# Optimization experiments

Measured on AMD Instinct MI355X. Metric: run time of the kernel, lower is better.

## Reference

```python
import jax, jax.numpy as jnp
import numpy as np

EPS = 1e-5
DN = ('NCHW', 'OIHW', 'NCHW')


def _conv3x3(x, w):
    return jax.lax.conv_general_dilated(x, w, (1, 1), 'SAME', dimension_numbers=DN)


def _bn_relu(x, g, b):
    # eval-mode BN: running_mean=0, running_var=1
    scale = (g / jnp.sqrt(1.0 + EPS))[None, :, None, None]
    return jax.nn.relu(x * scale + b[None, :, None, None])


def _double_conv(x, w1, g1, b1, w2, g2, b2):
    x = _bn_relu(_conv3x3(x, w1), g1, b1)
    return _bn_relu(_conv3x3(x, w2), g2, b2)


def _up2x_bilinear_align(x):
    # bilinear, align_corners=True, scale_factor=2
    def interp(a, axis, n_in):
        n_out = 2 * n_in
        pos = jnp.arange(n_out, dtype=jnp.float32) * (n_in - 1) / (n_out - 1)
        lo = jnp.floor(pos).astype(jnp.int32)
        hi = jnp.minimum(lo + 1, n_in - 1)
        w = pos - lo.astype(jnp.float32)
        sh = [1, 1, 1, 1]
        sh[axis] = n_out
        w = w.reshape(sh)
        return jnp.take(a, lo, axis=axis) * (1.0 - w) + jnp.take(a, hi, axis=axis) * w
    B, C, H, W = x.shape
    return interp(interp(x, 2, H), 3, W)


def _lstm_dir(seq, Wih, Whh, bih, bhh, reverse):
    # seq: (N, T, C) -> (N, T, Hh); PyTorch gate order i,f,g,o
    Hh = Whh.shape[1]
    xg = jnp.einsum('ntc,gc->ntg', seq, Wih) + (bih + bhh)
    if reverse:
        xg = xg[:, ::-1]
    xg = jnp.swapaxes(xg, 0, 1)  # (T, N, 4H)
    N = seq.shape[0]
    h0 = jnp.zeros((N, Hh), seq.dtype)

    def step(carry, gx):
        h, c = carry
        g = gx + h @ Whh.T
        i, f, gg, o = jnp.split(g, 4, axis=-1)
        c = jax.nn.sigmoid(f) * c + jax.nn.sigmoid(i) * jnp.tanh(gg)
        h = jax.nn.sigmoid(o) * jnp.tanh(c)
        return (h, c), h

    _, hs = jax.lax.scan(step, (h0, h0), xg)
    hs = jnp.swapaxes(hs, 0, 1)  # (N, T, Hh)
    if reverse:
        hs = hs[:, ::-1]
    return hs


def _bilstm(seq, Wf, Uf, bif, bhf, Wb, Ub, bib, bhb):
    return jnp.concatenate([
        _lstm_dir(seq, Wf, Uf, bif, bhf, False),
        _lstm_dir(seq, Wb, Ub, bib, bhb, True),
    ], axis=-1)


def _site_rows(x, lstm):
    # batched version of per-row LSTM: each row is a sequence over W, features C
    B, C, H, W = x.shape
    s = jnp.transpose(x, (0, 2, 3, 1)).reshape(B * H, W, C)
    out = _bilstm(s, *lstm)  # (B*H, W, C) since 2*hidden == C
    return jnp.transpose(out.reshape(B, H, W, C), (0, 3, 1, 2))


def _site_cols(x, lstm):
    # each column is a sequence over H, features C
    B, C, H, W = x.shape
    s = jnp.transpose(x, (0, 3, 2, 1)).reshape(B * W, H, C)
    out = _bilstm(s, *lstm)
    return jnp.transpose(out.reshape(B, W, H, C), (0, 3, 2, 1))


def setup_inputs() -> dict:
    key = jax.random.key(0)
    ks = jax.random.split(key, 24)
    d = {}
    d['x1'] = jax.random.normal(ks[0], (8, 128, 32, 32), jnp.float32)
    d['x2'] = jax.random.normal(ks[1], (8, 128, 64, 64), jnp.float32)
    # bidirectional LSTM: input 256, hidden 128
    d['lstm_Wih_f'] = jax.random.normal(ks[2], (512, 256), jnp.float32) * 0.06
    d['lstm_Whh_f'] = jax.random.normal(ks[3], (512, 128), jnp.float32) * 0.08
    d['lstm_bih_f'] = jax.random.normal(ks[4], (512,), jnp.float32) * 0.05
    d['lstm_bhh_f'] = jax.random.normal(ks[5], (512,), jnp.float32) * 0.05
    d['lstm_Wih_b'] = jax.random.normal(ks[6], (512, 256), jnp.float32) * 0.06
    d['lstm_Whh_b'] = jax.random.normal(ks[7], (512, 128), jnp.float32) * 0.08
    d['lstm_bib_tmp'] = None
    del d['lstm_bib_tmp']
    d['lstm_bih_b'] = jax.random.normal(ks[8], (512,), jnp.float32) * 0.05
    d['lstm_bhh_b'] = jax.random.normal(ks[9], (512,), jnp.float32) * 0.05
    # conv_2 = DoubleConv(512, 256) (mid=256), shared across its two call sites
    d['c2_w1'] = jax.random.normal(ks[10], (256, 512, 3, 3), jnp.float32) * 0.02
    d['c2_g1'] = jax.random.uniform(ks[11], (256,), jnp.float32, 0.5, 1.5)
    d['c2_b1'] = jax.random.normal(ks[12], (256,), jnp.float32) * 0.05
    d['c2_w2'] = jax.random.normal(ks[13], (256, 256, 3, 3), jnp.float32) * 0.03
    d['c2_g2'] = jax.random.uniform(ks[14], (256,), jnp.float32, 0.5, 1.5)
    d['c2_b2'] = jax.random.normal(ks[15], (256,), jnp.float32) * 0.05
    # conv = DoubleConv(256, 128, mid=128)
    d['cv_w1'] = jax.random.normal(ks[16], (128, 256, 3, 3), jnp.float32) * 0.03
    d['cv_g1'] = jax.random.uniform(ks[17], (128,), jnp.float32, 0.5, 1.5)
    d['cv_b1'] = jax.random.normal(ks[18], (128,), jnp.float32) * 0.05
    d['cv_w2'] = jax.random.normal(ks[19], (128, 128, 3, 3), jnp.float32) * 0.04
    d['cv_g2'] = jax.random.uniform(ks[20], (128,), jnp.float32, 0.5, 1.5)
    d['cv_b2'] = jax.random.normal(ks[21], (128,), jnp.float32) * 0.05
    return d


def reference(x1, x2, lstm_Wih_f, lstm_Whh_f, lstm_bih_f, lstm_bhh_f,
              lstm_Wih_b, lstm_Whh_b, lstm_bih_b, lstm_bhh_b,
              c2_w1, c2_g1, c2_b1, c2_w2, c2_g2, c2_b2,
              cv_w1, cv_g1, cv_b1, cv_w2, cv_g2, cv_b2):
    lstm = (lstm_Wih_f, lstm_Whh_f, lstm_bih_f, lstm_bhh_f,
            lstm_Wih_b, lstm_Whh_b, lstm_bih_b, lstm_bhh_b)
    x1u = _up2x_bilinear_align(x1)
    dy = x2.shape[2] - x1u.shape[2]
    dx = x2.shape[3] - x1u.shape[3]
    x1u = jnp.pad(x1u, ((0, 0), (0, 0), (dy // 2, dy - dy // 2), (dx // 2, dx - dx // 2)))
    x = jnp.concatenate([x2, x1u], axis=1)  # (B, 256, 64, 64)
    # site_relation mutates x in-place in torch: rows pass, then cols pass on the
    # row-updated tensor; x_weigth and x_heigth alias the same final tensor.
    x = _site_rows(x, lstm)
    x = _site_cols(x, lstm)
    x_site = jnp.concatenate([x, x], axis=1)  # (B, 512, H, W)
    x_site = _double_conv(x_site, c2_w1, c2_g1, c2_b1, c2_w2, c2_g2, c2_b2)
    x = jnp.concatenate([x, x_site], axis=1)  # (B, 512, H, W)
    x = _double_conv(x, c2_w1, c2_g1, c2_b1, c2_w2, c2_g2, c2_b2)
    x = _double_conv(x, cv_w1, cv_g1, cv_b1, cv_w2, cv_g2, cv_b2)
    return x  # (B, 128, 64, 64)
```

## Files before the change

### kernel.cpp

```cpp
#include <hip/hip_runtime.h>
#include <hip/hip_bf16.h>
#include <math.h>

typedef __bf16 bf16x8 __attribute__((ext_vector_type(8)));
typedef float  f32x4  __attribute__((ext_vector_type(4)));

__device__ __forceinline__ float sigm(float x)  { return 1.f/(1.f+__expf(-x)); }
__device__ __forceinline__ float tanh_f(float x){ return 2.f/(1.f+__expf(-2.f*x)) - 1.f; }
__device__ __forceinline__ float b2f(unsigned short u){
  unsigned int x = ((unsigned int)u) << 16; return __uint_as_float(x);
}
__device__ __forceinline__ unsigned short f2b(float v){
  __hip_bfloat16 h = __float2bfloat16(v); return *(unsigned short*)&h;
}
__device__ __forceinline__ void glds16(const void* g, void* l) {
  __builtin_amdgcn_global_load_lds(
      (const __attribute__((address_space(1))) unsigned int*)g,
      (__attribute__((address_space(3))) unsigned int*)l, 16, 0, 0);
}
__device__ __forceinline__ bf16x8 bzero() {
  bf16x8 v;
  #pragma unroll
  for (int i = 0; i < 8; ++i) v[i] = (__bf16)0.0f;
  return v;
}
__device__ __forceinline__ void barrier_lds() {
  asm volatile("s_waitcnt lgkmcnt(0)\n\ts_barrier" ::: "memory");
}

__global__ __launch_bounds__(256) void k_upcat(const float* __restrict__ x1,
                                               const float* __restrict__ x2,
                                               __hip_bfloat16* __restrict__ X0) {
  int idx = blockIdx.x*256 + threadIdx.x;
  int c = idx & 255;
  int w = (idx >> 8) & 63;
  int h = (idx >> 14) & 63;
  int n = idx >> 20;
  float v;
  if (c < 128) {
    v = x2[((n*128 + c)*64 + h)*64 + w];
  } else {
    int cc = c - 128;
    float py = (h*31.0f)/63.0f;
    int ly = (int)py; int hy = min(ly+1, 31); float fy = py - (float)ly;
    float px = (w*31.0f)/63.0f;
    int lx = (int)px; int hx = min(lx+1, 31); float fx = px - (float)lx;
    const float* p = x1 + (size_t)(n*128 + cc)*1024;
    float v00 = p[ly*32+lx], v01 = p[ly*32+hx];
    float v10 = p[hy*32+lx], v11 = p[hy*32+hx];
    v = (1.f-fy)*((1.f-fx)*v00 + fx*v01) + fy*((1.f-fx)*v10 + fx*v11);
  }
  X0[idx] = __float2bfloat16(v);
}

__global__ __launch_bounds__(256) void k_wih_prep(
    const float* __restrict__ Wf, const float* __restrict__ Wb,
    const float* __restrict__ bif, const float* __restrict__ bhf,
    const float* __restrict__ bib, const float* __restrict__ bhb,
    __hip_bfloat16* __restrict__ wihc, float* __restrict__ biasc) {
  int idx = blockIdx.x*256 + threadIdx.x;
  int n = idx >> 8, k = idx & 255;
  float v = (n < 512) ? Wf[n*256 + k] : Wb[(n-512)*256 + k];
  wihc[idx] = __float2bfloat16(v);
  if (idx < 1024) biasc[idx] = (idx < 512) ? bif[idx] + bhf[idx]
                                           : bib[idx-512] + bhb[idx-512];
}

__global__ __launch_bounds__(256) void k_xg_gemm(
    const __hip_bfloat16* __restrict__ Xin,
    const __hip_bfloat16* __restrict__ Wihc,
    const float* __restrict__ biasc,
    __hip_bfloat16* __restrict__ xg) {
  __shared__ __align__(16) unsigned short sa[128][72];
  __shared__ __align__(16) unsigned short sw[128][72];
  int bx = blockIdx.x;
  int t = bx >> 2, seq0 = (bx & 3) << 7;
  int n0 = blockIdx.y << 7;
  int tid = threadIdx.x, lane = tid & 63, wid = tid >> 6;
  int wm = wid >> 1, wn = wid & 1;
  int l15 = lane & 15, quad = lane >> 4;
  f32x4 acc[4][4];
  #pragma unroll
  for (int i = 0; i < 4; ++i)
    #pragma unroll
    for (int j = 0; j < 4; ++j) acc[i][j] = (f32x4){0.f,0.f,0.f,0.f};

  for (int k0 = 0; k0 < 256; k0 += 64) {
    __syncthreads();
    for (int idx = tid; idx < 2048; idx += 256) {
      int row = idx >> 4, c4 = (idx & 15) << 2;
      *(ushort4*)&sa[row][c4] = *(const ushort4*)((const unsigned short*)Xin +
          (size_t)((seq0 + row)*64 + t)*256 + k0 + c4);
      *(ushort4*)&sw[row][c4] = *(const ushort4*)((const unsigned short*)Wihc +
          (size_t)(n0 + row)*256 + k0 + c4);
    }
    __syncthreads();
    #pragma unroll
    for (int k32 = 0; k32 < 64; k32 += 32) {
      bf16x8 af[4], bfr[4];
      #pragma unroll
      for (int mt = 0; mt < 4; ++mt)
        af[mt] = *(const bf16x8*)&sa[wm*64 + mt*16 + l15][k32 + quad*8];
      #pragma unroll
      for (int nt = 0; nt < 4; ++nt)
        bfr[nt] = *(const bf16x8*)&sw[wn*64 + nt*16 + l15][k32 + quad*8];
      #pragma unroll
      for (int mt = 0; mt < 4; ++mt)
        #pragma unroll
        for (int nt = 0; nt < 4; ++nt)
          acc[mt][nt] = __builtin_amdgcn_mfma_f32_16x16x32_bf16(
              af[mt], bfr[nt], acc[mt][nt], 0, 0, 0);
    }
  }
  #pragma unroll
  for (int nt = 0; nt < 4; ++nt) {
    int cg = n0 + wn*64 + nt*16 + l15;
    int dir = cg >> 9;
    int g   = (cg >> 7) & 3;
    int u   = cg & 127;
    float bias = biasc[cg];
    unsigned short* op = (unsigned short*)xg +
        (size_t)(((dir*64 + t)*4 + g)*512)*128 + u;
    #pragma unroll
    for (int mt = 0; mt < 4; ++mt) {
      int sbase = seq0 + wm*64 + mt*16 + quad*4;
      f32x4 a = acc[mt][nt];
      #pragma unroll
      for (int r = 0; r < 4; ++r)
        op[(size_t)(sbase + r)*128] = f2b(a[r] + bias);
    }
  }
}

__global__ __launch_bounds__(256, 1) void k_lstm_rec(
    const __hip_bfloat16* __restrict__ xg,
    const float* __restrict__ WhhF, const float* __restrict__ WhhB,
    __hip_bfloat16* __restrict__ out) {
  const int dir = blockIdx.y;
  const int sb  = blockIdx.x;
  const float* Whh = dir ? WhhB : WhhF;
  __shared__ __align__(16) unsigned short hs[16][136];
  __shared__ __align__(16) float gv[4][128][4];
  const int tid = threadIdx.x, lane = tid & 63, wv = tid >> 6;
  const int l15 = lane & 15, quad = lane >> 4;

  bf16x8 wf[4][2][4];
  #pragma unroll
  for (int g = 0; g < 4; ++g)
    #pragma unroll
    for (int ut = 0; ut < 2; ++ut) {
      int gate = g*128 + wv*32 + ut*16 + l15;
      #pragma unroll
      for (int kc = 0; kc < 4; ++kc) {
        const float* wp = Whh + (size_t)gate*128 + kc*32 + quad*8;
        float4 w0 = *(const float4*)wp;
        float4 w1 = *(const float4*)(wp + 4);
        bf16x8 f;
        f[0]=(__bf16)w0.x; f[1]=(__bf16)w0.y; f[2]=(__bf16)w0.z; f[3]=(__bf16)w0.w;
        f[4]=(__bf16)w1.x; f[5]=(__bf16)w1.y; f[6]=(__bf16)w1.z; f[7]=(__bf16)w1.w;
        wf[g][ut][kc] = f;
      }
    }
  for (int i = tid; i < 16*136; i += 256) ((unsigned short*)hs)[i] = 0;

  const int u_  = tid & 127;
  const int s0_ = tid >> 7;
  float cst[2] = {0.f, 0.f};

  const unsigned short* xp = (const unsigned short*)xg +
      (size_t)dir*64*4*512*128;
  unsigned short xv[2][4], xn[2][4];
  #define LDX(stp, dst)                                                    \
    {                                                                      \
      int ts_ = (stp) < 64 ? (stp) : 63;                                   \
      int t_  = dir ? 63 - ts_ : ts_;                                      \
      _Pragma("unroll")                                                    \
      for (int j_ = 0; j_ < 2; ++j_) {                                     \
        int s_ = s0_ + j_*2;                                               \
        _Pragma("unroll")                                                  \
        for (int g_ = 0; g_ < 4; ++g_)                                     \
          dst[j_][g_] = xp[(size_t)((t_*4 + g_)*512 + sb*4 + s_)*128 + u_];\
      }                                                                    \
    }
  LDX(0, xv);
  __syncthreads();

  for (int step = 0; step < 64; ++step) {
    int t = dir ? 63 - step : step;
    LDX(step + 1, xn);
    bf16x8 af[2][4];
    #pragma unroll
    for (int mt = 0; mt < 2; ++mt)
      #pragma unroll
      for (int kc = 0; kc < 4; ++kc)
        af[mt][kc] = *(const bf16x8*)&hs[mt*16 + l15][kc*32 + quad*8];
    f32x4 acc[2][4][2];
    #pragma unroll
    for (int mt = 0; mt < 2; ++mt)
      #pragma unroll
      for (int g = 0; g < 4; ++g)
        #pragma unroll
        for (int ut = 0; ut < 2; ++ut) acc[mt][g][ut] = (f32x4){0.f,0.f,0.f,0.f};
    #pragma unroll
    for (int kc = 0; kc < 4; ++kc)
      #pragma unroll
      for (int mt = 0; mt < 2; ++mt)
        #pragma unroll
        for (int g = 0; g < 4; ++g)
          #pragma unroll
          for (int ut = 0; ut < 2; ++ut)
            acc[mt][g][ut] = __builtin_amdgcn_mfma_f32_16x16x32_bf16(
                af[mt][kc], wf[g][ut][kc], acc[mt][g][ut], 0, 0, 0);
    if (quad == 0) {
      #pragma unroll
      for (int ut = 0; ut < 2; ++ut) {
        int u = wv*32 + ut*16 + l15;
        #pragma unroll
        for (int r = 0; r < 4; ++r) {
          float4 q;
          q.x = acc[0][0][ut][r]; q.y = acc[0][1][ut][r];
          q.z = acc[0][2][ut][r]; q.w = acc[0][3][ut][r];
          *(float4*)&gv[r][u][0] = q;
        }
      }
    }
    barrier_lds();
    #pragma unroll
    for (int j = 0; j < 2; ++j) {
      int s = s0_ + j*2;
      float4 gq = *(const float4*)&gv[s][u_][0];
      float I = gq.x + b2f(xv[j][0]);
      float F = gq.y + b2f(xv[j][1]);
      float G = gq.z + b2f(xv[j][2]);
      float O = gq.w + b2f(xv[j][3]);
      float cv = sigm(F)*cst[j] + sigm(I)*tanh_f(G);
      float hv = sigm(O)*tanh_f(cv);
      cst[j] = cv;
      unsigned short hb = f2b(hv);
      hs[s][u_] = hb;
      int gs = sb*4 + s;
      ((unsigned short*)out)[(size_t)(((gs >> 6)*64 + t)*64 + (gs & 63))*256
                             + dir*128 + u_] = hb;
    }
    barrier_lds();
    #pragma unroll
    for (int j = 0; j < 2; ++j)
      #pragma unroll
      for (int g = 0; g < 4; ++g) xv[j][g] = xn[j][g];
  }
  #undef LDX
}

__global__ __launch_bounds__(256) void k_wrefmt_bf16(const float* __restrict__ src,
                                                     __hip_bfloat16* __restrict__ dst,
                                                     int Ci, int Co, int fold) {
  int idx = blockIdx.x*256 + threadIdx.x;
  int total = 9*Ci*Co;
  if (idx >= total) return;
  int ci = idx % Ci;
  int co = (idx / Ci) % Co;
  int k  = idx / (Ci*Co);
  int CiS = fold ? Ci*2 : Ci;
  float v = src[(size_t)(co*CiS + ci)*9 + k];
  if (fold) v += src[(size_t)(co*CiS + ci + Ci)*9 + k];
  dst[idx] = __float2bfloat16(v);
}

__global__ __launch_bounds__(256, 2) void k_conv3_v3(
    const __hip_bfloat16* __restrict__ inA, const __hip_bfloat16* __restrict__ inB,
    const __hip_bfloat16* __restrict__ wgt,
    const float* __restrict__ gam, const float* __restrict__ bet,
    float* __restrict__ outF, __hip_bfloat16* __restrict__ outB,
    int Cin, int Co, int nchw) {
  __shared__ __align__(16) unsigned short si[6][64][64];
  __shared__ __align__(16) unsigned short sw[3][64][64];
  int bx = blockIdx.x;
  int n  = bx >> 4;
  int h0 = (bx & 15) << 2;
  int co0 = blockIdx.y << 6;
  int tid = threadIdx.x;
  int lane = tid & 63;
  int wvid = tid >> 6;
  int l15 = lane & 15, quad = lane >> 4;
  int pl = lane >> 3, pc = lane & 7;

  f32x4 acc[4][4];
  #pragma unroll
  for (int i = 0; i < 4; ++i)
    #pragma unroll
    for (int j = 0; j < 4; ++j) acc[i][j] = (f32x4){0.f,0.f,0.f,0.f};

  int cs = inB ? 256 : Cin;
  for (int ci0 = 0; ci0 < Cin; ci0 += 64) {
    const unsigned short* src = (const unsigned short*)inA; int cb = ci0;
    if (inB && ci0 >= 256) { src = (const unsigned short*)inB; cb = ci0 - 256; }
    __syncthreads();
    #pragma unroll
    for (int j = 0; j < 12; ++j) {
      int s = wvid + j*4;
      int row = s >> 3, grp = s & 7;
      int ih = h0 + row - 1;
      if (ih >= 0 && ih <= 63) {
        const unsigned short* gsrc = src + (size_t)((n*64 + ih)*64)*cs + cb;
        int iw = grp*8 + pl;
        int lc = pc ^ (iw & 7);
        glds16(gsrc + (size_t)iw*cs + lc*8, &si[row][grp*8][0]);
      } else {
        uint4 z = {0,0,0,0};
        *(uint4*)((unsigned short*)&si[row][grp*8][0] + lane*8) = z;
      }
    }
    for (int ky = 0; ky < 3; ++ky) {
      if (ky) __syncthreads();
      {
        const unsigned short* wk = (const unsigned short*)wgt +
            (size_t)(ky*3*Co + co0)*Cin + ci0;
        #pragma unroll
        for (int j = 0; j < 6; ++j) {
          int s = wvid + j*4;
          int kx = s >> 3, cg = s & 7;
          int co = cg*8 + pl;
          int lc = pc ^ (co & 7);
          glds16(wk + (size_t)(kx*Co + co)*Cin + lc*8, &sw[kx][cg*8][0]);
        }
      }
      __syncthreads();
      int row = wvid + ky;
      #pragma unroll
      for (int kx = 0; kx < 3; ++kx) {
        #pragma unroll
        for (int k32 = 0; k32 < 2; ++k32) {
          bf16x8 af[4], bfr[4];
          #pragma unroll
          for (int mt = 0; mt < 4; ++mt) {
            int iw = mt*16 + l15 + kx - 1;
            int iwc = iw & 63;
            int pcc = (k32*4 + quad) ^ (iwc & 7);
            af[mt] = *(const bf16x8*)&si[row][iwc][pcc*8];
            if ((kx == 0 && mt == 0 && l15 == 0) ||
                (kx == 2 && mt == 3 && l15 == 15))
              af[mt] = bzero();
          }
          #pragma unroll
          for (int nt = 0; nt < 4; ++nt) {
            int co = nt*16 + l15;
            int pcc = (k32*4 + quad) ^ (co & 7);
            bfr[nt] = *(const bf16x8*)&sw[kx][co][pcc*8];
          }
          #pragma unroll
          for (int mt = 0; mt < 4; ++mt)
            #pragma unroll
            for (int nt = 0; nt < 4; ++nt)
              acc[mt][nt] = __builtin_amdgcn_mfma_f32_16x16x32_bf16(
                  af[mt], bfr[nt], acc[mt][nt], 0, 0, 0);
        }
      }
    }
  }
  const float kS = 0.9999950000374997f;
  int h = h0 + wvid;
  #pragma unroll
  for (int nt = 0; nt < 4; ++nt) {
    int co = co0 + nt*16 + l15;
    float scale = gam[co]*kS, bb = bet[co];
    #pragma unroll
    for (int mt = 0; mt < 4; ++mt) {
      f32x4 a = acc[mt][nt];
      #pragma unroll
      for (int r = 0; r < 4; ++r) {
        int w = mt*16 + quad*4 + r;
        float v = fmaf(a[r], scale, bb);
        v = v > 0.f ? v : 0.f;
        if (nchw) outF[(size_t)((n*Co + co)*64 + h)*64 + w] = v;
        else      outB[(size_t)((n*64 + h)*64 + w)*Co + co] = __float2bfloat16(v);
      }
    }
  }
}

extern "C" void kernel_launch(void* const* d_in, const int* in_sizes, int n_in,
                              void* d_out, int out_size, void* d_ws, size_t ws_size,
                              hipStream_t stream) {
  const float* x1    = (const float*)d_in[0];
  const float* x2    = (const float*)d_in[1];
  const float* Wih_f = (const float*)d_in[2];
  const float* Whh_f = (const float*)d_in[3];
  const float* bih_f = (const float*)d_in[4];
  const float* bhh_f = (const float*)d_in[5];
  const float* Wih_b = (const float*)d_in[6];
  const float* Whh_b = (const float*)d_in[7];
  const float* bih_b = (const float*)d_in[8];
  const float* bhh_b = (const float*)d_in[9];
  const float* c2_w1 = (const float*)d_in[10];
  const float* c2_g1 = (const float*)d_in[11];
  const float* c2_b1 = (const float*)d_in[12];
  const float* c2_w2 = (const float*)d_in[13];
  const float* c2_g2 = (const float*)d_in[14];
  const float* c2_b2 = (const float*)d_in[15];
  const float* cv_w1 = (const float*)d_in[16];
  const float* cv_g1 = (const float*)d_in[17];
  const float* cv_b1 = (const float*)d_in[18];
  const float* cv_w2 = (const float*)d_in[19];
  const float* cv_g2 = (const float*)d_in[20];
  const float* cv_b2 = (const float*)d_in[21];

  char* base = (char*)d_ws;
  const size_t SLOTB = 16777216ull;
  __hip_bfloat16* Xb  = (__hip_bfloat16*)(base);
  __hip_bfloat16* Sb  = (__hip_bfloat16*)(base);
  __hip_bfloat16* XG  = (__hip_bfloat16*)(base + SLOTB);
  __hip_bfloat16* D2  = (__hip_bfloat16*)(base + SLOTB);
  __hip_bfloat16* D2b = (__hip_bfloat16*)(base + 2*SLOTB);
  __hip_bfloat16* RT  = (__hip_bfloat16*)(base + SLOTB + 67108864ull);
  __hip_bfloat16* D1  = RT;
  char* wq = base + SLOTB + 67108864ull + SLOTB;
  __hip_bfloat16* wihc  = (__hip_bfloat16*)wq;
  float*          biasc = (float*)(wq + 524288);
  char* cw = wq + 528384;
  __hip_bfloat16* w1f    = (__hip_bfloat16*)(cw);
  __hip_bfloat16* w1full = (__hip_bfloat16*)(cw + 1179648);
  __hip_bfloat16* w2r    = (__hip_bfloat16*)(cw + 3538944);
  __hip_bfloat16* wv1    = (__hip_bfloat16*)(cw + 4718592);
  __hip_bfloat16* wv2    = (__hip_bfloat16*)(cw + 5308416);

  k_wih_prep<<<1024, 256, 0, stream>>>(Wih_f, Wih_b, bih_f, bhh_f, bih_b, bhh_b,
                                       wihc, biasc);
  k_wrefmt_bf16<<<(9*256*256+255)/256, 256, 0, stream>>>(c2_w1, w1f,    256, 256, 1);
  k_wrefmt_bf16<<<(9*512*256+255)/256, 256, 0, stream>>>(c2_w1, w1full, 512, 256, 0);
  k_wrefmt_bf16<<<(9*256*256+255)/256, 256, 0, stream>>>(c2_w2, w2r,    256, 256, 0);
  k_wrefmt_bf16<<<(9*256*128+255)/256, 256, 0, stream>>>(cv_w1, wv1,    256, 128, 0);
  k_wrefmt_bf16<<<(9*128*128+255)/256, 256, 0, stream>>>(cv_w2, wv2,    128, 128, 0);

  k_upcat<<<32768, 256, 0, stream>>>(x1, x2, Xb);

  k_xg_gemm<<<dim3(256, 8), 256, 0, stream>>>(Xb, wihc, biasc, XG);
  k_lstm_rec<<<dim3(128, 2), 256, 0, stream>>>(XG, Whh_f, Whh_b, RT);
  k_xg_gemm<<<dim3(256, 8), 256, 0, stream>>>(RT, wihc, biasc, XG);
  k_lstm_rec<<<dim3(128, 2), 256, 0, stream>>>(XG, Whh_f, Whh_b, Sb);

  k_conv3_v3<<<dim3(128,4), 256, 0, stream>>>(Sb, nullptr, w1f, c2_g1, c2_b1,
                                              nullptr, D1, 256, 256, 0);
  k_conv3_v3<<<dim3(128,4), 256, 0, stream>>>(D1, nullptr, w2r, c2_g2, c2_b2,
                                              nullptr, D2, 256, 256, 0);
  k_conv3_v3<<<dim3(128,4), 256, 0, stream>>>(Sb, D2, w1full, c2_g1, c2_b1,
                                              nullptr, D2b, 512, 256, 0);
  k_conv3_v3<<<dim3(128,4), 256, 0, stream>>>(D2b, nullptr, w2r, c2_g2, c2_b2,
                                              nullptr, D1, 256, 256, 0);
  k_conv3_v3<<<dim3(128,2), 256, 0, stream>>>(D1, nullptr, wv1, cv_g1, cv_b1,
                                              nullptr, D2, 256, 128, 0);
  k_conv3_v3<<<dim3(128,2), 256, 0, stream>>>(D2, nullptr, wv2, cv_g2, cv_b2,
                                              (float*)d_out, nullptr, 128, 128, 1);
}
```

Baseline: 656.8 us.

## Restructure LSTM recurrence: 16 sequences per block, transposed MFMA, double-buffered h

The recurrent LSTM kernel now handles 16 sequences per block instead of 4, so the grid shrinks from 128x2 to 32x2. The MFMA is transposed (weights as the A operand, h as B), which leaves each lane holding all four gate values for its units. The gate nonlinearities can then run straight from registers, with the input projection preloaded into the accumulator, dropping the LDS gate staging and one barrier per step. h is double-buffered in LDS so a single barrier per step suffices. The cost is fewer blocks (64 total) and therefore less parallelism on the device.

```diff
diff --git a/kernel.cpp b/kernel.cpp
--- a/kernel.cpp
+++ b/kernel.cpp
@@ -139,116 +139,116 @@
   const int dir = blockIdx.y;
   const int sb  = blockIdx.x;
   const float* Whh = dir ? WhhB : WhhF;
-  __shared__ __align__(16) unsigned short hs[16][136];
-  __shared__ __align__(16) float gv[4][128][4];
+  __shared__ __align__(16) unsigned short hs[2][16][136];
   const int tid = threadIdx.x, lane = tid & 63, wv = tid >> 6;
   const int l15 = lane & 15, quad = lane >> 4;
 
-  bf16x8 wf[4][2][4];
-  #pragma unroll
-  for (int g = 0; g < 4; ++g)
-    #pragma unroll
-    for (int ut = 0; ut < 2; ++ut) {
-      int gate = g*128 + wv*32 + ut*16 + l15;
+  bf16x8 wf[2][4][4];
+  #pragma unroll
+  for (int mt = 0; mt < 2; ++mt)
+    #pragma unroll
+    for (int g = 0; g < 4; ++g) {
+      int row = g*128 + wv*32 + mt*16 + l15;
       #pragma unroll
       for (int kc = 0; kc < 4; ++kc) {
-        const float* wp = Whh + (size_t)gate*128 + kc*32 + quad*8;
+        const float* wp = Whh + (size_t)row*128 + kc*32 + quad*8;
         float4 w0 = *(const float4*)wp;
         float4 w1 = *(const float4*)(wp + 4);
         bf16x8 f;
         f[0]=(__bf16)w0.x; f[1]=(__bf16)w0.y; f[2]=(__bf16)w0.z; f[3]=(__bf16)w0.w;
         f[4]=(__bf16)w1.x; f[5]=(__bf16)w1.y; f[6]=(__bf16)w1.z; f[7]=(__bf16)w1.w;
-        wf[g][ut][kc] = f;
+        wf[mt][g][kc] = f;
       }
     }
   for (int i = tid; i < 16*136; i += 256) ((unsigned short*)hs)[i] = 0;
 
-  const int u_  = tid & 127;
-  const int s0_ = tid >> 7;
-  float cst[2] = {0.f, 0.f};
-
+  const int seq = l15;
+  int xoff[2][4];
+  #pragma unroll
+  for (int mt = 0; mt < 2; ++mt)
+    #pragma unroll
+    for (int g = 0; g < 4; ++g)
+      xoff[mt][g] = ((g*512) + sb*16 + seq)*128 + wv*32 + mt*16 + quad*4;
   const unsigned short* xp = (const unsigned short*)xg +
       (size_t)dir*64*4*512*128;
-  unsigned short xv[2][4], xn[2][4];
-  #define LDX(stp, dst)                                                    \
-    {                                                                      \
-      int ts_ = (stp) < 64 ? (stp) : 63;                                   \
-      int t_  = dir ? 63 - ts_ : ts_;                                      \
-      _Pragma("unroll")                                                    \
-      for (int j_ = 0; j_ < 2; ++j_) {                                     \
-        int s_ = s0_ + j_*2;                                               \
-        _Pragma("unroll")                                                  \
-        for (int g_ = 0; g_ < 4; ++g_)                                     \
-          dst[j_][g_] = xp[(size_t)((t_*4 + g_)*512 + sb*4 + s_)*128 + u_];\
-      }                                                                    \
-    }
-  LDX(0, xv);
+  const int gs = sb*16 + seq;
+  unsigned short* outb = (unsigned short*)out +
+      ((size_t)(gs >> 6)*64)*64*256 + (size_t)(gs & 63)*256 + dir*128;
+
+  ushort4 xv[2][4], xn[2][4];
+  {
+    int t0 = dir ? 63 : 0;
+    const unsigned short* bt = xp + (size_t)t0*262144;
+    #pragma unroll
+    for (int mt = 0; mt < 2; ++mt)
+      #pragma unroll
+      for (int g = 0; g < 4; ++g)
+        xv[mt][g] = *(const ushort4*)(bt + xoff[mt][g]);
+  }
+  float cst[2][4];
+  #pragma unroll
+  for (int mt = 0; mt < 2; ++mt)
+    #pragma unroll
+    for (int r = 0; r < 4; ++r) cst[mt][r] = 0.f;
   __syncthreads();
 
-  for (int step = 0; step < 64; ++step) {
+  auto body = [&](int step, ushort4 (&xc)[2][4], ushort4 (&xf)[2][4]) {
     int t = dir ? 63 - step : step;
-    LDX(step + 1, xn);
-    bf16x8 af[2][4];
-    #pragma unroll
-    for (int mt = 0; mt < 2; ++mt)
-      #pragma unroll
-      for (int kc = 0; kc < 4; ++kc)
-        af[mt][kc] = *(const bf16x8*)&hs[mt*16 + l15][kc*32 + quad*8];
-    f32x4 acc[2][4][2];
-    #pragma unroll
-    for (int mt = 0; mt < 2; ++mt)
-      #pragma unroll
-      for (int g = 0; g < 4; ++g)
-        #pragma unroll
-        for (int ut = 0; ut < 2; ++ut) acc[mt][g][ut] = (f32x4){0.f,0.f,0.f,0.f};
-    #pragma unroll
-    for (int kc = 0; kc < 4; ++kc)
+    {
+      int sn = step + 1 < 64 ? step + 1 : 63;
+      int tn = dir ? 63 - sn : sn;
+      const unsigned short* bt = xp + (size_t)tn*262144;
       #pragma unroll
       for (int mt = 0; mt < 2; ++mt)
         #pragma unroll
         for (int g = 0; g < 4; ++g)
-          #pragma unroll
-          for (int ut = 0; ut < 2; ++ut)
-            acc[mt][g][ut] = __builtin_amdgcn_mfma_f32_16x16x32_bf16(
-                af[mt][kc], wf[g][ut][kc], acc[mt][g][ut], 0, 0, 0);
-    if (quad == 0) {
-      #pragma unroll
-      for (int ut = 0; ut < 2; ++ut) {
-        int u = wv*32 + ut*16 + l15;
+          xf[mt][g] = *(const ushort4*)(bt + xoff[mt][g]);
+    }
+    const int cur = step & 1;
+    bf16x8 hf[4];
+    #pragma unroll
+    for (int kc = 0; kc < 4; ++kc)
+      hf[kc] = *(const bf16x8*)&hs[cur][l15][kc*32 + quad*8];
+    f32x4 acc[2][4];
+    #pragma unroll
+    for (int mt = 0; mt < 2; ++mt)
+      #pragma unroll
+      for (int g = 0; g < 4; ++g) {
+        acc[mt][g][0] = b2f(xc[mt][g].x);
+        acc[mt][g][1] = b2f(xc[mt][g].y);
+        acc[mt][g][2] = b2f(xc[mt][g].z);
+        acc[mt][g][3] = b2f(xc[mt][g].w);
+      }
+    #pragma unroll
+    for (int kc = 0; kc < 4; ++kc)
+      #pragma unroll
+      for (int mt = 0; mt < 2; ++mt)
         #pragma unroll
-        for (int r = 0; r < 4; ++r) {
-          float4 q;
-          q.x = acc[0][0][ut][r]; q.y = acc[0][1][ut][r];
-          q.z = acc[0][2][ut][r]; q.w = acc[0][3][ut][r];
-          *(float4*)&gv[r][u][0] = q;
-        }
-      }
+        for (int g = 0; g < 4; ++g)
+          acc[mt][g] = __builtin_amdgcn_mfma_f32_16x16x32_bf16(
+              wf[mt][g][kc], hf[kc], acc[mt][g], 0, 0, 0);
+    #pragma unroll
+    for (int mt = 0; mt < 2; ++mt) {
+      ushort4 hb;
+      #pragma unroll
+      for (int r = 0; r < 4; ++r) {
+        float I = acc[mt][0][r], F = acc[mt][1][r];
+        float G = acc[mt][2][r], O = acc[mt][3][r];
+        float cv = sigm(F)*cst[mt][r] + sigm(I)*tanh_f(G);
+        float hv = sigm(O)*tanh_f(cv);
+        cst[mt][r] = cv;
+        ((unsigned short*)&hb)[r] = f2b(hv);
+      }
+      int u = wv*32 + mt*16 + quad*4;
+      *(ushort4*)&hs[cur ^ 1][l15][u] = hb;
+      *(ushort4*)(outb + (size_t)t*16384 + u) = hb;
     }
     barrier_lds();
-    #pragma unroll
-    for (int j = 0; j < 2; ++j) {
-      int s = s0_ + j*2;
-      float4 gq = *(const float4*)&gv[s][u_][0];
-      float I = gq.x + b2f(xv[j][0]);
-      float F = gq.y + b2f(xv[j][1]);
-      float G = gq.z + b2f(xv[j][2]);
-      float O = gq.w + b2f(xv[j][3]);
-      float cv = sigm(F)*cst[j] + sigm(I)*tanh_f(G);
-      float hv = sigm(O)*tanh_f(cv);
-      cst[j] = cv;
-      unsigned short hb = f2b(hv);
-      hs[s][u_] = hb;
-      int gs = sb*4 + s;
-      ((unsigned short*)out)[(size_t)(((gs >> 6)*64 + t)*64 + (gs & 63))*256
-                             + dir*128 + u_] = hb;
-    }
-    barrier_lds();
-    #pragma unroll
-    for (int j = 0; j < 2; ++j)
-      #pragma unroll
-      for (int g = 0; g < 4; ++g) xv[j][g] = xn[j][g];
-  }
-  #undef LDX
+  };
+  for (int step = 0; step < 64; step += 2) {
+    body(step,     xv, xn);
+    body(step + 1, xn, xv);
+  }
 }
 
 __global__ __launch_bounds__(256) void k_wrefmt_bf16(const float* __restrict__ src,
@@ -434,9 +434,9 @@
   k_upcat<<<32768, 256, 0, stream>>>(x1, x2, Xb);
 
   k_xg_gemm<<<dim3(256, 8), 256, 0, stream>>>(Xb, wihc, biasc, XG);
-  k_lstm_rec<<<dim3(128, 2), 256, 0, stream>>>(XG, Whh_f, Whh_b, RT);
+  k_lstm_rec<<<dim3(32, 2), 256, 0, stream>>>(XG, Whh_f, Whh_b, RT);
   k_xg_gemm<<<dim3(256, 8), 256, 0, stream>>>(RT, wihc, biasc, XG);
-  k_lstm_rec<<<dim3(128, 2), 256, 0, stream>>>(XG, Whh_f, Whh_b, Sb);
+  k_lstm_rec<<<dim3(32, 2), 256, 0, stream>>>(XG, Whh_f, Whh_b, Sb);
 
   k_conv3_v3<<<dim3(128,4), 256, 0, stream>>>(Sb, nullptr, w1f, c2_g1, c2_b1,
                                               nullptr, D1, 256, 256, 0);
```

New measurement: 831.5 us. +26.6%, slower.
